# Kernel optimization log

Hardware: AMD Instinct MI355X
Metric: run time of the kernel (lower is better)

The kernel has to match this reference:

```python
import jax, jax.numpy as jnp
import numpy as np

T = 0.04
PIC_NUM = 4  # images per identity (hardcoded in SP_loss)


def setup_inputs() -> dict:
    key = jax.random.key(0)
    N, D = 8192, 256  # 2048 identities x 4 images, 256-dim ReID features
    x = jax.random.normal(key, (N, D), dtype=jnp.float32)
    x = x / jnp.linalg.norm(x, axis=1, keepdims=True)  # L2-normalize (cosine sims)
    return {"x": x}


def reference(x):
    N = x.shape[0]
    G = N // PIC_NUM  # number of identity groups
    s = (x @ x.T) / T  # [N, N] scaled similarity matrix

    # Diagonal 4x4 blocks: within-class similarities. [G, 4, 4]
    d4 = s.reshape(G, PIC_NUM, G, PIC_NUM)
    gidx = jnp.arange(G)
    pos = d4[gidx, :, gidx, :]  # [G, 4, 4]

    # hard positive: -T * log( sum_{i,j in class} exp(-dot_ij / T) )  (soft-min)
    hard_pos = -T * jax.nn.logsumexp(-pos.reshape(G, PIC_NUM * PIC_NUM), axis=1)

    # least-hard positive: T * log( sum_i 1 / (sum_j exp(-dot_ij / T)) )
    lse_row = jax.nn.logsumexp(-pos, axis=2)           # [G, 4] = log sum_j exp(-dot/T)
    least_pos = T * jax.nn.logsumexp(-lse_row, axis=1)  # [G]

    # negatives: T * log( sum_{i in class, j not in class} exp(dot_ij / T) )
    col_group = jnp.arange(N) // PIC_NUM              # [N]
    same = col_group[None, :] == gidx[:, None]        # [G, N] same-class column mask
    s3 = s.reshape(G, PIC_NUM, N)
    neg_masked = jnp.where(same[:, None, :], -jnp.inf, s3)
    neg = T * jax.nn.logsumexp(neg_masked.reshape(G, PIC_NUM * N), axis=1)  # [G]

    # Original detaches all three S vectors before forming the loss.
    hard_pos = jax.lax.stop_gradient(hard_pos)
    least_pos = jax.lax.stop_gradient(least_pos)
    neg = jax.lax.stop_gradient(neg)

    # alpha: harmonic mean of (hard, least-hard) when hard >= 0, else 0
    alpha = jnp.where(hard_pos >= 0.0,
                      2.0 * least_pos * hard_pos / (hard_pos + least_pos),
                      0.0)
    margin = alpha * hard_pos + (1.0 - alpha) * least_pos
    # log(1 + exp(z)) == softplus(z), numerically stable, same math
    loss = jnp.mean(jax.nn.softplus((neg - margin) / T))
    return loss
```

## Files before the change

kernel.cpp:

```cpp
#include <hip/hip_runtime.h>
#include <math.h>


#define NROWS 8192
#define DDIM  256
#define NGRP  2048
#define NTB   128
#define NTILES (NTB * (NTB + 1) / 2)
#define TPW   2
#define NWAVES (NTILES / TPW)
#define WPB   4
#define NWG   (NWAVES / WPB)
#define T_CONST 0.04f
#define INV_T   25.0f
#define QSCALE  5.0f
#define SCALE_ONE 0x7F7F7F7Fu

typedef __attribute__((ext_vector_type(8))) int   i32x8_t;
typedef __attribute__((ext_vector_type(4))) float f32x4_t;

__global__ __launch_bounds__(256) void prep_kernel(const float* __restrict__ x,
                                                   unsigned int* __restrict__ xq,
                                                   float* __restrict__ margin,
                                                   float* __restrict__ out) {
    const int b = blockIdx.x;
    if (b < 512) {
        if (b == 0 && threadIdx.x == 0) out[0] = 0.f;
#pragma unroll
        for (int it = 0; it < 4; ++it) {
            int gid = it * 131072 + b * 256 + threadIdx.x;
            float4 v = *(const float4*)(x + (size_t)gid * 4);
            int pk = __builtin_amdgcn_cvt_pk_fp8_f32(v.x * QSCALE, v.y * QSCALE, 0, false);
            pk = __builtin_amdgcn_cvt_pk_fp8_f32(v.z * QSCALE, v.w * QSCALE, pk, true);
            xq[gid] = (unsigned int)pk;
        }
        return;
    }
    const int g = (b - 512) * 4 + (threadIdx.x >> 6);
    const int lane = threadIdx.x & 63;
    const float* xr = x + (size_t)g * 4 * DDIM;
    float4 v0 = *(const float4*)(xr + 4 * lane);
    float4 v1 = *(const float4*)(xr + DDIM + 4 * lane);
    float4 v2 = *(const float4*)(xr + 2 * DDIM + 4 * lane);
    float4 v3 = *(const float4*)(xr + 3 * DDIM + 4 * lane);
    float4 vv[4] = {v0, v1, v2, v3};
    float a[16];
#pragma unroll
    for (int i = 0; i < 4; ++i)
#pragma unroll
        for (int j = 0; j < 4; ++j) {
            float d = vv[i].x * vv[j].x + vv[i].y * vv[j].y
                    + vv[i].z * vv[j].z + vv[i].w * vv[j].w;
            a[i * 4 + j] = d;
        }
#pragma unroll
    for (int k = 0; k < 16; ++k) {
        float t = a[k];
        t += __shfl_xor(t, 32, 64);
        t += __shfl_xor(t, 16, 64);
        t += __shfl_xor(t, 8, 64);
        t += __shfl_xor(t, 4, 64);
        t += __shfl_xor(t, 2, 64);
        t += __shfl_xor(t, 1, 64);
        a[k] = t;
    }
    if (lane == 0) {
        float pos[16];
#pragma unroll
        for (int k = 0; k < 16; ++k) pos[k] = a[k] * INV_T;

        float mx = -pos[0];
#pragma unroll
        for (int k = 1; k < 16; ++k) mx = fmaxf(mx, -pos[k]);
        float se = 0.f;
#pragma unroll
        for (int k = 0; k < 16; ++k) se += __expf(-pos[k] - mx);
        float hard_pos = -T_CONST * (mx + __logf(se));

        float lse_row[4];
#pragma unroll
        for (int i = 0; i < 4; ++i) {
            float m2 = -pos[i * 4];
#pragma unroll
            for (int j = 1; j < 4; ++j) m2 = fmaxf(m2, -pos[i * 4 + j]);
            float s2 = 0.f;
#pragma unroll
            for (int j = 0; j < 4; ++j) s2 += __expf(-pos[i * 4 + j] - m2);
            lse_row[i] = m2 + __logf(s2);
        }
        float m3 = -lse_row[0];
#pragma unroll
        for (int i = 1; i < 4; ++i) m3 = fmaxf(m3, -lse_row[i]);
        float s3 = 0.f;
#pragma unroll
        for (int i = 0; i < 4; ++i) s3 += __expf(-lse_row[i] - m3);
        float least_pos = T_CONST * (m3 + __logf(s3));

        float alpha = (hard_pos >= 0.f)
                          ? (2.f * least_pos * hard_pos) / (hard_pos + least_pos)
                          : 0.f;
        margin[g] = alpha * hard_pos + (1.f - alpha) * least_pos;
    }
}

__global__ __launch_bounds__(256) void gemm_exp_contrib(const unsigned char* __restrict__ xq,
                                                        float* __restrict__ contrib) {
    const int waveId = threadIdx.x >> 6;
    const int idx0 = (blockIdx.x * WPB + waveId) * TPW;
    int ti = (int)((257.0f - sqrtf(66049.0f - 8.0f * (float)idx0)) * 0.5f);
    while (ti * (257 - ti) / 2 > idx0) --ti;
    while ((ti + 1) * (256 - ti) / 2 <= idx0) ++ti;
    int tj = ti + (idx0 - ti * (257 - ti) / 2);

    const int lane = threadIdx.x & 63;
    const int quad = lane >> 4;
    const int l16 = lane & 15;

    int voff[8];
#pragma unroll
    for (int z = 0; z < 8; ++z)
        voff[z] = (((z & 3) * 16 + l16) << 8) + (z >> 2) * 128 + quad * 32;

    i32x8_t aF[2][4];
    int curTi = -1;

    int runTi = ti, runTj = tj;
    bool isStart = true;
    float rowgAcc[4] = {0.f, 0.f, 0.f, 0.f};

    for (int t = 0; t < TPW; ++t) {
        const bool diag = (ti == tj);

        if (ti != curTi) {
            curTi = ti;
            const unsigned char* ab = xq + ((size_t)ti << 14);
#pragma unroll
            for (int z = 0; z < 8; ++z)
                aF[z >> 2][z & 3] = *(const i32x8_t*)(ab + voff[z]);
        }

        i32x8_t bF[2][4];
        {
            const unsigned char* bb = xq + ((size_t)tj << 14);
#pragma unroll
            for (int z = 0; z < 8; ++z)
                bF[z >> 2][z & 3] = *(const i32x8_t*)(bb + voff[z]);
        }

        f32x4_t acc[4][4];
#pragma unroll
        for (int i = 0; i < 4; ++i)
#pragma unroll
            for (int j = 0; j < 4; ++j)
                acc[i][j] = (f32x4_t){0.f, 0.f, 0.f, 0.f};

#pragma unroll
        for (int ks = 0; ks < 2; ++ks)
#pragma unroll
            for (int mi = 0; mi < 4; ++mi)
#pragma unroll
                for (int ni = 0; ni < 4; ++ni)
                    acc[mi][ni] = __builtin_amdgcn_mfma_scale_f32_16x16x128_f8f6f4(
                        aF[ks][mi], bF[ks][ni], acc[mi][ni],
                        0, 0,
                        0, (int)SCALE_ONE,
                        0, (int)SCALE_ONE);

        float colp[4] = {0.f, 0.f, 0.f, 0.f};
        if (!diag) {
#pragma unroll
            for (int mi = 0; mi < 4; ++mi)
#pragma unroll
                for (int ni = 0; ni < 4; ++ni) {
                    float s4 = __expf(acc[mi][ni][0]) + __expf(acc[mi][ni][1])
                             + __expf(acc[mi][ni][2]) + __expf(acc[mi][ni][3]);
                    rowgAcc[mi] += s4;
                    colp[ni] += s4;
                }
        } else {
#pragma unroll
            for (int mi = 0; mi < 4; ++mi) {
                const int rgrp = mi * 4 + quad;
#pragma unroll
                for (int ni = 0; ni < 4; ++ni) {
                    const int cgrp = ni * 4 + (l16 >> 2);
                    if (cgrp != rgrp) {
                        float s4 = __expf(acc[mi][ni][0]) + __expf(acc[mi][ni][1])
                                 + __expf(acc[mi][ni][2]) + __expf(acc[mi][ni][3]);
                        rowgAcc[mi] += s4;
                    }
                }
            }
        }

        if (!isStart && l16 == 0) {
            float* crow = contrib + (((size_t)ti * NTB + tj) << 4);
#pragma unroll
            for (int mi = 0; mi < 4; ++mi) crow[mi * 4 + quad] = 0.f;
        }

        if (!diag) {
            float* ccol = contrib + (((size_t)tj * NTB + ti) << 4);
#pragma unroll
            for (int ni = 0; ni < 4; ++ni) {
                float v = colp[ni];
                v += __shfl_xor(v, 16, 64);
                v += __shfl_xor(v, 32, 64);
                v += __shfl_xor(v, 1, 64);
                v += __shfl_xor(v, 2, 64);
                if (quad == 0 && (l16 & 3) == 0) ccol[ni * 4 + (l16 >> 2)] = v;
            }
        }

        int nti = ti, ntj = tj + 1;
        if (ntj == NTB) { ++nti; ntj = nti; }
        const bool flush = (t == TPW - 1) || (nti != runTi);
        if (flush) {
            float* crow = contrib + (((size_t)runTi * NTB + runTj) << 4);
#pragma unroll
            for (int mi = 0; mi < 4; ++mi) {
                float v = rowgAcc[mi];
                v += __shfl_xor(v, 1, 64);
                v += __shfl_xor(v, 2, 64);
                v += __shfl_xor(v, 4, 64);
                v += __shfl_xor(v, 8, 64);
                if (l16 == 0) crow[mi * 4 + quad] = v;
                rowgAcc[mi] = 0.f;
            }
            runTi = nti; runTj = ntj;
            isStart = true;
        } else {
            isStart = false;
        }
        ti = nti; tj = ntj;
    }
}

__global__ __launch_bounds__(256) void finalize_kernel(const float* __restrict__ contrib,
                                                       const float* __restrict__ margin,
                                                       float* __restrict__ out) {
    const int tid = threadIdx.x;
    const int g = blockIdx.x * 256 + tid;
    const int p = g >> 4;
    const int idx = g & 15;
    const float* base = contrib + (((size_t)p * NTB) << 4) + idx;
    float s = 0.f;
#pragma unroll 4
    for (int q = 0; q < NTB; ++q) s += base[(size_t)q << 4];
    float z = __logf(s) - margin[g] * INV_T;
    float local = (z > 30.f) ? z : log1pf(__expf(z));

    local += __shfl_xor(local, 1, 64);
    local += __shfl_xor(local, 2, 64);
    local += __shfl_xor(local, 4, 64);
    local += __shfl_xor(local, 8, 64);
    local += __shfl_xor(local, 16, 64);
    local += __shfl_xor(local, 32, 64);
    __shared__ float wsum[4];
    if ((tid & 63) == 0) wsum[tid >> 6] = local;
    __syncthreads();
    if (tid == 0)
        atomicAdd(out, (wsum[0] + wsum[1] + wsum[2] + wsum[3]) * (1.f / (float)NGRP));
}

extern "C" void kernel_launch(void* const* d_in, const int* in_sizes, int n_in,
                              void* d_out, int out_size, void* d_ws, size_t ws_size,
                              hipStream_t stream) {
    const float* x = (const float*)d_in[0];
    float* out = (float*)d_out;

    unsigned int* xq = (unsigned int*)d_ws;
    float* contrib = (float*)((char*)d_ws + (size_t)NROWS * DDIM);
    float* margin = contrib + (size_t)NTB * NTB * 16;

    prep_kernel<<<1024, 256, 0, stream>>>(x, xq, margin, out);
    gemm_exp_contrib<<<NWG, 256, 0, stream>>>((const unsigned char*)xq, contrib);
    finalize_kernel<<<8, 256, 0, stream>>>(contrib, margin, out);
}
```

Baseline: 105.2 us.

## Software-pipeline MFMA halves with exp epilogue and prefetch next tile per wave

Splits each 64x64 tile's MFMA work into two column halves with double-buffered accumulators. The exp/reduction epilogue of the previous half runs while the MFMAs of the current half are in flight, and the next tile's fragments are prefetched early. It also launches one wave per workgroup instead of four, and drops the zero-fill path for rows that are not flushed by writing each tile's row partial directly. The aim is to overlap transcendental work with matrix work and to hide load latency, at the cost of higher register pressure and more workgroups to schedule.

After: 110.1 us. +4.7%, slower.

```diff
diff --git a/kernel.cpp b/kernel.cpp
--- a/kernel.cpp
+++ b/kernel.cpp
@@ -8,9 +8,7 @@
 #define NTB   128
 #define NTILES (NTB * (NTB + 1) / 2)
 #define TPW   2
-#define NWAVES (NTILES / TPW)
-#define WPB   4
-#define NWG   (NWAVES / WPB)
+#define NWG   (NTILES / TPW)
 #define T_CONST 0.04f
 #define INV_T   25.0f
 #define QSCALE  5.0f
@@ -48,11 +46,9 @@
 #pragma unroll
     for (int i = 0; i < 4; ++i)
 #pragma unroll
-        for (int j = 0; j < 4; ++j) {
-            float d = vv[i].x * vv[j].x + vv[i].y * vv[j].y
-                    + vv[i].z * vv[j].z + vv[i].w * vv[j].w;
-            a[i * 4 + j] = d;
-        }
+        for (int j = 0; j < 4; ++j)
+            a[i * 4 + j] = vv[i].x * vv[j].x + vv[i].y * vv[j].y
+                         + vv[i].z * vv[j].z + vv[i].w * vv[j].w;
 #pragma unroll
     for (int k = 0; k < 16; ++k) {
         float t = a[k];
@@ -103,136 +99,175 @@
     }
 }
 
-__global__ __launch_bounds__(256) void gemm_exp_contrib(const unsigned char* __restrict__ xq,
-                                                        float* __restrict__ contrib) {
-    const int waveId = threadIdx.x >> 6;
-    const int idx0 = (blockIdx.x * WPB + waveId) * TPW;
+__global__ __launch_bounds__(64) void gemm_exp_contrib(const unsigned char* __restrict__ xq,
+                                                       float* __restrict__ contrib) {
+    const int idx0 = blockIdx.x * TPW;
     int ti = (int)((257.0f - sqrtf(66049.0f - 8.0f * (float)idx0)) * 0.5f);
     while (ti * (257 - ti) / 2 > idx0) --ti;
     while ((ti + 1) * (256 - ti) / 2 <= idx0) ++ti;
     int tj = ti + (idx0 - ti * (257 - ti) / 2);
 
-    const int lane = threadIdx.x & 63;
+    const int lane = threadIdx.x;
     const int quad = lane >> 4;
     const int l16 = lane & 15;
+    const int cgsub = l16 >> 2;
 
     int voff[8];
 #pragma unroll
     for (int z = 0; z < 8; ++z)
         voff[z] = (((z & 3) * 16 + l16) << 8) + (z >> 2) * 128 + quad * 32;
 
-    i32x8_t aF[2][4];
-    int curTi = -1;
-
-    int runTi = ti, runTj = tj;
-    bool isStart = true;
-    float rowgAcc[4] = {0.f, 0.f, 0.f, 0.f};
-
+    i32x8_t aF[2][4], bF[2][4];
+    {
+        const unsigned char* ab = xq + ((size_t)ti << 14);
+        const unsigned char* bb = xq + ((size_t)tj << 14);
+#pragma unroll
+        for (int z = 0; z < 8; ++z) {
+            aF[z >> 2][z & 3] = *(const i32x8_t*)(ab + voff[z]);
+            bF[z >> 2][z & 3] = *(const i32x8_t*)(bb + voff[z]);
+        }
+    }
+
+    f32x4_t accD[2][4][2];
+    float rowg[4] = {0.f, 0.f, 0.f, 0.f};
+
+    int eTi = 0, eTj = 0, eNh = 0, eBuf = 0;
+    bool eDiag = false, pending = false;
+
+#pragma unroll
     for (int t = 0; t < TPW; ++t) {
         const bool diag = (ti == tj);
-
-        if (ti != curTi) {
-            curTi = ti;
-            const unsigned char* ab = xq + ((size_t)ti << 14);
-#pragma unroll
-            for (int z = 0; z < 8; ++z)
-                aF[z >> 2][z & 3] = *(const i32x8_t*)(ab + voff[z]);
-        }
-
-        i32x8_t bF[2][4];
-        {
-            const unsigned char* bb = xq + ((size_t)tj << 14);
-#pragma unroll
-            for (int z = 0; z < 8; ++z)
-                bF[z >> 2][z & 3] = *(const i32x8_t*)(bb + voff[z]);
-        }
-
-        f32x4_t acc[4][4];
-#pragma unroll
-        for (int i = 0; i < 4; ++i)
-#pragma unroll
-            for (int j = 0; j < 4; ++j)
-                acc[i][j] = (f32x4_t){0.f, 0.f, 0.f, 0.f};
-
-#pragma unroll
-        for (int ks = 0; ks < 2; ++ks)
+        const int cTi = ti, cTj = tj;
+
+#pragma unroll
+        for (int nh = 0; nh < 2; ++nh) {
+            const int buf = nh;
 #pragma unroll
             for (int mi = 0; mi < 4; ++mi)
 #pragma unroll
-                for (int ni = 0; ni < 4; ++ni)
-                    acc[mi][ni] = __builtin_amdgcn_mfma_scale_f32_16x16x128_f8f6f4(
-                        aF[ks][mi], bF[ks][ni], acc[mi][ni],
-                        0, 0,
-                        0, (int)SCALE_ONE,
-                        0, (int)SCALE_ONE);
-
-        float colp[4] = {0.f, 0.f, 0.f, 0.f};
-        if (!diag) {
-#pragma unroll
-            for (int mi = 0; mi < 4; ++mi)
-#pragma unroll
-                for (int ni = 0; ni < 4; ++ni) {
-                    float s4 = __expf(acc[mi][ni][0]) + __expf(acc[mi][ni][1])
-                             + __expf(acc[mi][ni][2]) + __expf(acc[mi][ni][3]);
-                    rowgAcc[mi] += s4;
-                    colp[ni] += s4;
-                }
-        } else {
-#pragma unroll
-            for (int mi = 0; mi < 4; ++mi) {
-                const int rgrp = mi * 4 + quad;
-#pragma unroll
-                for (int ni = 0; ni < 4; ++ni) {
-                    const int cgrp = ni * 4 + (l16 >> 2);
-                    if (cgrp != rgrp) {
-                        float s4 = __expf(acc[mi][ni][0]) + __expf(acc[mi][ni][1])
-                                 + __expf(acc[mi][ni][2]) + __expf(acc[mi][ni][3]);
-                        rowgAcc[mi] += s4;
+                for (int nj = 0; nj < 2; ++nj)
+                    accD[buf][mi][nj] = (f32x4_t){0.f, 0.f, 0.f, 0.f};
+#pragma unroll
+            for (int ks = 0; ks < 2; ++ks)
+#pragma unroll
+                for (int mi = 0; mi < 4; ++mi)
+#pragma unroll
+                    for (int nj = 0; nj < 2; ++nj)
+                        accD[buf][mi][nj] = __builtin_amdgcn_mfma_scale_f32_16x16x128_f8f6f4(
+                            aF[ks][mi], bF[ks][nh * 2 + nj], accD[buf][mi][nj],
+                            0, 0,
+                            0, (int)SCALE_ONE,
+                            0, (int)SCALE_ONE);
+
+            if (nh == 1 && t + 1 < TPW) {
+                int nti = ti, ntj = tj + 1;
+                if (ntj == NTB) { ++nti; ntj = nti; }
+                const unsigned char* bb = xq + ((size_t)ntj << 14);
+#pragma unroll
+                for (int z = 0; z < 8; ++z)
+                    bF[z >> 2][z & 3] = *(const i32x8_t*)(bb + voff[z]);
+                if (nti != ti) {
+                    const unsigned char* ab = xq + ((size_t)nti << 14);
+#pragma unroll
+                    for (int z = 0; z < 8; ++z)
+                        aF[z >> 2][z & 3] = *(const i32x8_t*)(ab + voff[z]);
+                }
+                ti = nti; tj = ntj;
+            }
+
+            if (pending) {
+                float colp[2] = {0.f, 0.f};
+#pragma unroll
+                for (int mi = 0; mi < 4; ++mi) {
+                    const int rgrp = mi * 4 + quad;
+#pragma unroll
+                    for (int nj = 0; nj < 2; ++nj) {
+                        const f32x4_t av = accD[eBuf][mi][nj];
+                        float s4 = __expf(av[0]) + __expf(av[1])
+                                 + __expf(av[2]) + __expf(av[3]);
+                        if (eDiag) {
+                            const int cgrp = (eNh * 2 + nj) * 4 + cgsub;
+                            if (cgrp != rgrp) rowg[mi] += s4;
+                        } else {
+                            rowg[mi] += s4;
+                            colp[nj] += s4;
+                        }
                     }
                 }
+                if (!eDiag) {
+                    float* ccol = contrib + (((size_t)eTj * NTB + eTi) << 4);
+#pragma unroll
+                    for (int nj = 0; nj < 2; ++nj) {
+                        float v = colp[nj];
+                        v += __shfl_xor(v, 16, 64);
+                        v += __shfl_xor(v, 32, 64);
+                        v += __shfl_xor(v, 1, 64);
+                        v += __shfl_xor(v, 2, 64);
+                        if (quad == 0 && (l16 & 3) == 0)
+                            ccol[(eNh * 2 + nj) * 4 + cgsub] = v;
+                    }
+                }
+                if (eNh == 1) {
+                    float* crow = contrib + (((size_t)eTi * NTB + eTj) << 4);
+#pragma unroll
+                    for (int mi = 0; mi < 4; ++mi) {
+                        float v = rowg[mi];
+                        v += __shfl_xor(v, 1, 64);
+                        v += __shfl_xor(v, 2, 64);
+                        v += __shfl_xor(v, 4, 64);
+                        v += __shfl_xor(v, 8, 64);
+                        if (l16 == 0) crow[mi * 4 + quad] = v;
+                        rowg[mi] = 0.f;
+                    }
+                }
             }
-        }
-
-        if (!isStart && l16 == 0) {
-            float* crow = contrib + (((size_t)ti * NTB + tj) << 4);
-#pragma unroll
-            for (int mi = 0; mi < 4; ++mi) crow[mi * 4 + quad] = 0.f;
-        }
-
-        if (!diag) {
-            float* ccol = contrib + (((size_t)tj * NTB + ti) << 4);
-#pragma unroll
-            for (int ni = 0; ni < 4; ++ni) {
-                float v = colp[ni];
+            eTi = cTi; eTj = cTj; eNh = nh; eBuf = buf; eDiag = diag;
+            pending = true;
+        }
+    }
+
+    {
+        float colp[2] = {0.f, 0.f};
+#pragma unroll
+        for (int mi = 0; mi < 4; ++mi) {
+            const int rgrp = mi * 4 + quad;
+#pragma unroll
+            for (int nj = 0; nj < 2; ++nj) {
+                const f32x4_t av = accD[eBuf][mi][nj];
+                float s4 = __expf(av[0]) + __expf(av[1])
+                         + __expf(av[2]) + __expf(av[3]);
+                if (eDiag) {
+                    const int cgrp = (eNh * 2 + nj) * 4 + cgsub;
+                    if (cgrp != rgrp) rowg[mi] += s4;
+                } else {
+                    rowg[mi] += s4;
+                    colp[nj] += s4;
+                }
+            }
+        }
+        if (!eDiag) {
+            float* ccol = contrib + (((size_t)eTj * NTB + eTi) << 4);
+#pragma unroll
+            for (int nj = 0; nj < 2; ++nj) {
+                float v = colp[nj];
                 v += __shfl_xor(v, 16, 64);
                 v += __shfl_xor(v, 32, 64);
                 v += __shfl_xor(v, 1, 64);
                 v += __shfl_xor(v, 2, 64);
-                if (quad == 0 && (l16 & 3) == 0) ccol[ni * 4 + (l16 >> 2)] = v;
+                if (quad == 0 && (l16 & 3) == 0)
+                    ccol[(eNh * 2 + nj) * 4 + cgsub] = v;
             }
         }
-
-        int nti = ti, ntj = tj + 1;
-        if (ntj == NTB) { ++nti; ntj = nti; }
-        const bool flush = (t == TPW - 1) || (nti != runTi);
-        if (flush) {
-            float* crow = contrib + (((size_t)runTi * NTB + runTj) << 4);
-#pragma unroll
-            for (int mi = 0; mi < 4; ++mi) {
-                float v = rowgAcc[mi];
-                v += __shfl_xor(v, 1, 64);
-                v += __shfl_xor(v, 2, 64);
-                v += __shfl_xor(v, 4, 64);
-                v += __shfl_xor(v, 8, 64);
-                if (l16 == 0) crow[mi * 4 + quad] = v;
-                rowgAcc[mi] = 0.f;
-            }
-            runTi = nti; runTj = ntj;
-            isStart = true;
-        } else {
-            isStart = false;
-        }
-        ti = nti; tj = ntj;
+        float* crow = contrib + (((size_t)eTi * NTB + eTj) << 4);
+#pragma unroll
+        for (int mi = 0; mi < 4; ++mi) {
+            float v = rowg[mi];
+            v += __shfl_xor(v, 1, 64);
+            v += __shfl_xor(v, 2, 64);
+            v += __shfl_xor(v, 4, 64);
+            v += __shfl_xor(v, 8, 64);
+            if (l16 == 0) crow[mi * 4 + quad] = v;
+        }
     }
 }
 
@@ -274,6 +309,6 @@
     float* margin = contrib + (size_t)NTB * NTB * 16;
 
     prep_kernel<<<1024, 256, 0, stream>>>(x, xq, margin, out);
-    gemm_exp_contrib<<<NWG, 256, 0, stream>>>((const unsigned char*)xq, contrib);
+    gemm_exp_contrib<<<NWG, 64, 0, stream>>>((const unsigned char*)xq, contrib);
     finalize_kernel<<<8, 256, 0, stream>>>(contrib, margin, out);
 }
```

## Process one tile per wave with split-K fragment loads and higher occupancy

Applied to the files above, without the earlier changes.

Each wave now computes a single 64x64 tile of the symmetric similarity matrix instead of two consecutive tiles. This removes the A-fragment reuse, the running row accumulator and the flush/zero bookkeeping. Fragments are loaded per K-half instead of all at once, and launch bounds request 3 workgroups per CU, which cuts register pressure so more waves can hide load latency. The cost is twice as many waves, no A reuse across tiles, and one row write per tile.

Measured after the change: 111.1 us. 1.06x slower.

```diff
diff --git a/kernel.cpp b/kernel.cpp
--- a/kernel.cpp
+++ b/kernel.cpp
@@ -7,10 +7,8 @@
 #define NGRP  2048
 #define NTB   128
 #define NTILES (NTB * (NTB + 1) / 2)
-#define TPW   2
-#define NWAVES (NTILES / TPW)
 #define WPB   4
-#define NWG   (NWAVES / WPB)
+#define NWG   (NTILES / WPB)
 #define T_CONST 0.04f
 #define INV_T   25.0f
 #define QSCALE  5.0f
@@ -48,11 +46,9 @@
 #pragma unroll
     for (int i = 0; i < 4; ++i)
 #pragma unroll
-        for (int j = 0; j < 4; ++j) {
-            float d = vv[i].x * vv[j].x + vv[i].y * vv[j].y
-                    + vv[i].z * vv[j].z + vv[i].w * vv[j].w;
-            a[i * 4 + j] = d;
-        }
+        for (int j = 0; j < 4; ++j)
+            a[i * 4 + j] = vv[i].x * vv[j].x + vv[i].y * vv[j].y
+                         + vv[i].z * vv[j].z + vv[i].w * vv[j].w;
 #pragma unroll
     for (int k = 0; k < 16; ++k) {
         float t = a[k];
@@ -103,136 +99,104 @@
     }
 }
 
-__global__ __launch_bounds__(256) void gemm_exp_contrib(const unsigned char* __restrict__ xq,
-                                                        float* __restrict__ contrib) {
+__global__ __launch_bounds__(256, 3) void gemm_exp_contrib(const unsigned char* __restrict__ xq,
+                                                           float* __restrict__ contrib) {
     const int waveId = threadIdx.x >> 6;
-    const int idx0 = (blockIdx.x * WPB + waveId) * TPW;
-    int ti = (int)((257.0f - sqrtf(66049.0f - 8.0f * (float)idx0)) * 0.5f);
-    while (ti * (257 - ti) / 2 > idx0) --ti;
-    while ((ti + 1) * (256 - ti) / 2 <= idx0) ++ti;
-    int tj = ti + (idx0 - ti * (257 - ti) / 2);
+    const int idx = blockIdx.x * WPB + waveId;
+    int ti = (int)((257.0f - sqrtf(66049.0f - 8.0f * (float)idx)) * 0.5f);
+    while (ti * (257 - ti) / 2 > idx) --ti;
+    while ((ti + 1) * (256 - ti) / 2 <= idx) ++ti;
+    const int tj = ti + (idx - ti * (257 - ti) / 2);
+    const bool diag = (ti == tj);
 
     const int lane = threadIdx.x & 63;
     const int quad = lane >> 4;
     const int l16 = lane & 15;
+    const int cgsub = l16 >> 2;
 
     int voff[8];
 #pragma unroll
     for (int z = 0; z < 8; ++z)
         voff[z] = (((z & 3) * 16 + l16) << 8) + (z >> 2) * 128 + quad * 32;
 
-    i32x8_t aF[2][4];
-    int curTi = -1;
-
-    int runTi = ti, runTj = tj;
-    bool isStart = true;
-    float rowgAcc[4] = {0.f, 0.f, 0.f, 0.f};
-
-    for (int t = 0; t < TPW; ++t) {
-        const bool diag = (ti == tj);
-
-        if (ti != curTi) {
-            curTi = ti;
-            const unsigned char* ab = xq + ((size_t)ti << 14);
-#pragma unroll
-            for (int z = 0; z < 8; ++z)
-                aF[z >> 2][z & 3] = *(const i32x8_t*)(ab + voff[z]);
-        }
-
-        i32x8_t bF[2][4];
-        {
-            const unsigned char* bb = xq + ((size_t)tj << 14);
-#pragma unroll
-            for (int z = 0; z < 8; ++z)
-                bF[z >> 2][z & 3] = *(const i32x8_t*)(bb + voff[z]);
-        }
-
-        f32x4_t acc[4][4];
-#pragma unroll
-        for (int i = 0; i < 4; ++i)
-#pragma unroll
-            for (int j = 0; j < 4; ++j)
-                acc[i][j] = (f32x4_t){0.f, 0.f, 0.f, 0.f};
-
-#pragma unroll
-        for (int ks = 0; ks < 2; ++ks)
-#pragma unroll
-            for (int mi = 0; mi < 4; ++mi)
-#pragma unroll
-                for (int ni = 0; ni < 4; ++ni)
-                    acc[mi][ni] = __builtin_amdgcn_mfma_scale_f32_16x16x128_f8f6f4(
-                        aF[ks][mi], bF[ks][ni], acc[mi][ni],
-                        0, 0,
-                        0, (int)SCALE_ONE,
-                        0, (int)SCALE_ONE);
-
-        float colp[4] = {0.f, 0.f, 0.f, 0.f};
-        if (!diag) {
-#pragma unroll
-            for (int mi = 0; mi < 4; ++mi)
-#pragma unroll
-                for (int ni = 0; ni < 4; ++ni) {
+    const unsigned char* ab = xq + ((size_t)ti << 14);
+    const unsigned char* bb = xq + ((size_t)tj << 14);
+
+    f32x4_t acc[4][4];
+#pragma unroll
+    for (int i = 0; i < 4; ++i)
+#pragma unroll
+        for (int j = 0; j < 4; ++j)
+            acc[i][j] = (f32x4_t){0.f, 0.f, 0.f, 0.f};
+
+#pragma unroll
+    for (int ks = 0; ks < 2; ++ks) {
+        i32x8_t aF[4], bF[4];
+#pragma unroll
+        for (int i = 0; i < 4; ++i) {
+            aF[i] = *(const i32x8_t*)(ab + voff[ks * 4 + i]);
+            bF[i] = *(const i32x8_t*)(bb + voff[ks * 4 + i]);
+        }
+#pragma unroll
+        for (int mi = 0; mi < 4; ++mi)
+#pragma unroll
+            for (int ni = 0; ni < 4; ++ni)
+                acc[mi][ni] = __builtin_amdgcn_mfma_scale_f32_16x16x128_f8f6f4(
+                    aF[mi], bF[ni], acc[mi][ni],
+                    0, 0,
+                    0, (int)SCALE_ONE,
+                    0, (int)SCALE_ONE);
+    }
+
+    float rowg[4] = {0.f, 0.f, 0.f, 0.f};
+    float colp[4] = {0.f, 0.f, 0.f, 0.f};
+    if (!diag) {
+#pragma unroll
+        for (int mi = 0; mi < 4; ++mi)
+#pragma unroll
+            for (int ni = 0; ni < 4; ++ni) {
+                float s4 = __expf(acc[mi][ni][0]) + __expf(acc[mi][ni][1])
+                         + __expf(acc[mi][ni][2]) + __expf(acc[mi][ni][3]);
+                rowg[mi] += s4;
+                colp[ni] += s4;
+            }
+    } else {
+#pragma unroll
+        for (int mi = 0; mi < 4; ++mi) {
+            const int rgrp = mi * 4 + quad;
+#pragma unroll
+            for (int ni = 0; ni < 4; ++ni) {
+                const int cgrp = ni * 4 + cgsub;
+                if (cgrp != rgrp) {
                     float s4 = __expf(acc[mi][ni][0]) + __expf(acc[mi][ni][1])
                              + __expf(acc[mi][ni][2]) + __expf(acc[mi][ni][3]);
-                    rowgAcc[mi] += s4;
-                    colp[ni] += s4;
-                }
-        } else {
-#pragma unroll
-            for (int mi = 0; mi < 4; ++mi) {
-                const int rgrp = mi * 4 + quad;
-#pragma unroll
-                for (int ni = 0; ni < 4; ++ni) {
-                    const int cgrp = ni * 4 + (l16 >> 2);
-                    if (cgrp != rgrp) {
-                        float s4 = __expf(acc[mi][ni][0]) + __expf(acc[mi][ni][1])
-                                 + __expf(acc[mi][ni][2]) + __expf(acc[mi][ni][3]);
-                        rowgAcc[mi] += s4;
-                    }
+                    rowg[mi] += s4;
                 }
             }
         }
-
-        if (!isStart && l16 == 0) {
-            float* crow = contrib + (((size_t)ti * NTB + tj) << 4);
-#pragma unroll
-            for (int mi = 0; mi < 4; ++mi) crow[mi * 4 + quad] = 0.f;
-        }
-
-        if (!diag) {
-            float* ccol = contrib + (((size_t)tj * NTB + ti) << 4);
-#pragma unroll
-            for (int ni = 0; ni < 4; ++ni) {
-                float v = colp[ni];
-                v += __shfl_xor(v, 16, 64);
-                v += __shfl_xor(v, 32, 64);
-                v += __shfl_xor(v, 1, 64);
-                v += __shfl_xor(v, 2, 64);
-                if (quad == 0 && (l16 & 3) == 0) ccol[ni * 4 + (l16 >> 2)] = v;
-            }
-        }
-
-        int nti = ti, ntj = tj + 1;
-        if (ntj == NTB) { ++nti; ntj = nti; }
-        const bool flush = (t == TPW - 1) || (nti != runTi);
-        if (flush) {
-            float* crow = contrib + (((size_t)runTi * NTB + runTj) << 4);
-#pragma unroll
-            for (int mi = 0; mi < 4; ++mi) {
-                float v = rowgAcc[mi];
-                v += __shfl_xor(v, 1, 64);
-                v += __shfl_xor(v, 2, 64);
-                v += __shfl_xor(v, 4, 64);
-                v += __shfl_xor(v, 8, 64);
-                if (l16 == 0) crow[mi * 4 + quad] = v;
-                rowgAcc[mi] = 0.f;
-            }
-            runTi = nti; runTj = ntj;
-            isStart = true;
-        } else {
-            isStart = false;
-        }
-        ti = nti; tj = ntj;
+    }
+
+    float* crow = contrib + (((size_t)ti * NTB + tj) << 4);
+#pragma unroll
+    for (int mi = 0; mi < 4; ++mi) {
+        float v = rowg[mi];
+        v += __shfl_xor(v, 1, 64);
+        v += __shfl_xor(v, 2, 64);
+        v += __shfl_xor(v, 4, 64);
+        v += __shfl_xor(v, 8, 64);
+        if (l16 == 0) crow[mi * 4 + quad] = v;
+    }
+    if (!diag) {
+        float* ccol = contrib + (((size_t)tj * NTB + ti) << 4);
+#pragma unroll
+        for (int ni = 0; ni < 4; ++ni) {
+            float v = colp[ni];
+            v += __shfl_xor(v, 16, 64);
+            v += __shfl_xor(v, 32, 64);
+            v += __shfl_xor(v, 1, 64);
+            v += __shfl_xor(v, 2, 64);
+            if (quad == 0 && (l16 & 3) == 0) ccol[ni * 4 + cgsub] = v;
+        }
     }
 }
 
```
